# Kernel optimization log

Measured on AMD Instinct MI355X. Metric: run time of the kernel, lower is better.

Reference implementation:

```python
import jax, jax.numpy as jnp
import numpy as np

B, T, D = 128, 512, 400
N_VALS, N_ACTS = 1024, 128

def setup_inputs() -> dict:
    key = jax.random.key(0)
    ks = jax.random.split(key, 7)
    H_utt = jax.random.normal(ks[0], (B, T, D), dtype=jnp.float32)
    c_utt = jax.random.normal(ks[1], (B, D), dtype=jnp.float32)
    C_acts = jax.random.normal(ks[2], (B, N_ACTS, D), dtype=jnp.float32)
    C_vals = jax.random.normal(ks[3], (N_VALS, 1, D), dtype=jnp.float32)
    W_score = jax.random.normal(ks[4], (1, D), dtype=jnp.float32) * (1.0 / np.sqrt(D))
    b_score = jnp.zeros((1,), dtype=jnp.float32)
    lens = jax.random.randint(ks[5], (B,), T // 2, T + 1, dtype=jnp.int64 if jax.config.read('jax_enable_x64') else jnp.int32)
    lens = lens.at[0].set(T)  # ensure max(lens) == T so masking matches torch semantics
    return {"H_utt": H_utt, "c_utt": c_utt, "C_acts": C_acts, "C_vals": C_vals,
            "W_score": W_score, "b_score": b_score, "utterance_len": lens}

def reference(H_utt, c_utt, C_acts, C_vals, W_score, b_score, utterance_len):
    vals = C_vals[:, 0, :]                                   # [V, D]
    # --- y_utts: default attention of each value vector over utterance states ---
    scores = jnp.einsum('btd,vd->bvt', H_utt, vals)          # mul+sum scoring
    mask = jnp.arange(T)[None, :] < utterance_len[:, None]   # [B, T]
    scores = jnp.where(mask[:, None, :], scores, -jnp.inf)
    probs = jax.nn.softmax(scores, axis=-1)                  # [B, V, T]
    q_utts = jnp.einsum('bvt,btd->bvd', probs, H_utt)        # weighted sum contexts
    y_utts = jnp.einsum('bvd,d->bv', q_utts, W_score[0]) + b_score[0]  # utt_scorer
    # --- y_acts: attention of c_utt over per-example act vectors, then score vs vals ---
    s2 = jnp.einsum('bad,bd->ba', C_acts, c_utt)
    p2 = jax.nn.softmax(s2, axis=-1)
    q_acts = jnp.einsum('ba,bad->bd', p2, C_acts)            # [B, D]
    y_acts = q_acts @ vals.T                                 # [B, V]
    return (y_utts, y_acts)
```

## Files before the change

### kernel.cpp

```cpp
#include <hip/hip_runtime.h>
#include <hip/hip_bf16.h>

#define B_  128
#define T_  512
#define D_  400
#define NV  1024
#define NA  128

#define LDH  424
#define NT   32
#define MV   128

typedef __bf16 bf16_t;
typedef bf16_t bf16x8 __attribute__((ext_vector_type(8)));
typedef bf16_t bf16x4 __attribute__((ext_vector_type(4)));
typedef float  floatx4 __attribute__((ext_vector_type(4)));

__device__ inline void async_copy16(const void* g, void* l) {
    __builtin_amdgcn_global_load_lds(
        (const __attribute__((address_space(1))) unsigned int*)g,
        (__attribute__((address_space(3))) unsigned int*)l, 16, 0, 0);
}

__device__ inline float dot4(float4 a, float4 b) {
    return a.x * b.x + a.y * b.y + a.z * b.z + a.w * b.w;
}

__global__ __launch_bounds__(256) void hw_prep_kernel(const float* __restrict__ H,
                                                      const float* __restrict__ W,
                                                      float* __restrict__ hw,
                                                      bf16_t* __restrict__ Hbf) {
    int wave = threadIdx.x >> 6;
    int lane = threadIdx.x & 63;
    long row = (long)blockIdx.x * 4 + wave;
    const float* h = H + row * D_;
    bf16_t* orow = Hbf + row * (long)LDH;
    float acc = 0.f;
    if (lane < 50) {
        const float4* p  = (const float4*)(h + lane * 8);
        const float4* wp = (const float4*)(W + lane * 8);
        float4 x = p[0], y = p[1];
        float4 wx = wp[0], wy = wp[1];
        acc = dot4(x, wx) + dot4(y, wy);
        bf16x8 f;
        f[0] = (bf16_t)x.x; f[1] = (bf16_t)x.y; f[2] = (bf16_t)x.z; f[3] = (bf16_t)x.w;
        f[4] = (bf16_t)y.x; f[5] = (bf16_t)y.y; f[6] = (bf16_t)y.z; f[7] = (bf16_t)y.w;
        *(bf16x8*)(orow + lane * 8) = f;
    } else if (lane < 53) {
        bf16x8 z;
#pragma unroll
        for (int j = 0; j < 8; ++j) z[j] = (bf16_t)0.0f;
        *(bf16x8*)(orow + 400 + (lane - 50) * 8) = z;
    }
#pragma unroll
    for (int off = 1; off < 64; off <<= 1) acc += __shfl_xor(acc, off, 64);
    if (lane == 0) hw[row] = acc;
}

__global__ __launch_bounds__(256) void hw_kernel(const float* __restrict__ H,
                                                 const float* __restrict__ W,
                                                 float* __restrict__ hw) {
    int wave = threadIdx.x >> 6;
    int lane = threadIdx.x & 63;
    long row = (long)blockIdx.x * 4 + wave;
    const float* h = H + row * D_;
    float acc = 0.f;
    for (int k = lane; k < D_; k += 64) acc += h[k] * W[k];
#pragma unroll
    for (int off = 1; off < 64; off <<= 1) acc += __shfl_xor(acc, off, 64);
    if (lane == 0) hw[row] = acc;
}

__global__ __launch_bounds__(256) void qacts_kernel(const float* __restrict__ cu,
                                                    const float* __restrict__ Ca,
                                                    float* __restrict__ q_ws) {
    __shared__ __align__(16) float4 cu4[100];
    __shared__ float s_lds[NA];
    __shared__ float p_lds[NA];
    __shared__ float red[8];
    __shared__ __align__(16) float4 part[100];
    int b = blockIdx.x;
    int tid = threadIdx.x, wave = tid >> 6, lane = tid & 63;

    if (tid < 100) cu4[tid] = ((const float4*)(cu + (size_t)b * D_))[tid];
    __syncthreads();

    const float4* Cb4 = (const float4*)(Ca + (size_t)b * NA * D_);
#pragma unroll 2
    for (int i = 0; i < 32; ++i) {
        int a = wave * 32 + i;
        const float4* row = Cb4 + (size_t)a * 100;
        float acc = dot4(row[lane], cu4[lane]);
        if (lane < 36) acc += dot4(row[lane + 64], cu4[lane + 64]);
#pragma unroll
        for (int off = 1; off < 64; off <<= 1) acc += __shfl_xor(acc, off, 64);
        if (lane == 0) s_lds[a] = acc;
    }
    __syncthreads();

    float s = (tid < NA) ? s_lds[tid] : -3.0e38f;
    float m = s;
#pragma unroll
    for (int off = 1; off < 64; off <<= 1) m = fmaxf(m, __shfl_xor(m, off, 64));
    if (lane == 0) red[wave] = m;
    __syncthreads();
    m = fmaxf(red[0], red[1]);
    float e = (tid < NA) ? __expf(s - m) : 0.f;
    float sum = e;
#pragma unroll
    for (int off = 1; off < 64; off <<= 1) sum += __shfl_xor(sum, off, 64);
    if (lane == 0) red[4 + wave] = sum;
    __syncthreads();
    float S = red[4] + red[5];
    if (tid < NA) p_lds[tid] = e / S;
    __syncthreads();

    int c4 = tid % 100;
    int half = tid / 100;
    float4 acc0 = {0.f, 0.f, 0.f, 0.f};
    if (tid < 200) {
        float4 acc1 = {0.f, 0.f, 0.f, 0.f};
        int a0 = half * 64;
#pragma unroll 4
        for (int a = 0; a < 64; a += 2) {
            float p0 = p_lds[a0 + a], p1 = p_lds[a0 + a + 1];
            float4 x0 = Cb4[(size_t)(a0 + a) * 100 + c4];
            float4 x1 = Cb4[(size_t)(a0 + a + 1) * 100 + c4];
            acc0.x += p0 * x0.x; acc0.y += p0 * x0.y; acc0.z += p0 * x0.z; acc0.w += p0 * x0.w;
            acc1.x += p1 * x1.x; acc1.y += p1 * x1.y; acc1.z += p1 * x1.z; acc1.w += p1 * x1.w;
        }
        acc0.x += acc1.x; acc0.y += acc1.y; acc0.z += acc1.z; acc0.w += acc1.w;
        if (half == 1) part[c4] = acc0;
    }
    __syncthreads();
    if (tid < 100) {
        float4 o = part[c4];
        o.x += acc0.x; o.y += acc0.y; o.z += acc0.z; o.w += acc0.w;
        ((float4*)(q_ws + (size_t)b * D_))[c4] = o;
    }
}

template<int PRE>
__global__ __launch_bounds__(256, 2) void main_kernel(const float* __restrict__ H,
                                                      const bf16_t* __restrict__ Hbf,
                                                      const float* __restrict__ Cv,
                                                      const float* __restrict__ hw,
                                                      const float* __restrict__ q_ws,
                                                      const float* __restrict__ bs,
                                                      const int* __restrict__ lens,
                                                      float* __restrict__ out) {
    __shared__ bf16_t h_lds[2][NT * LDH];

    int i = blockIdx.x;
    int xcd = i & 7, vc = (i >> 3) & 7, bb = i >> 6;
    int b = xcd + 8 * bb;
    int vbase = vc * MV;

    int tid = threadIdx.x;
    int wave = tid >> 6, lane = tid & 63;
    int lrow = lane & 15, quad = lane >> 4;

    int len = lens[b];
    float b0 = bs[0];

    if (!PRE) {
        for (int idx = tid; idx < 2 * NT * (LDH - D_); idx += 256) {
            int bu = idx / (NT * (LDH - D_));
            int rem = idx % (NT * (LDH - D_));
            int r = rem / (LDH - D_), c = rem % (LDH - D_);
            h_lds[bu][r * LDH + D_ + c] = (bf16_t)0.0f;
        }
    }

    bf16x8 afrag[2][13];
#pragma unroll
    for (int set = 0; set < 2; ++set) {
        const float* vrow = Cv + (size_t)(vbase + wave * 32 + set * 16 + lrow) * D_;
#pragma unroll
        for (int kk = 0; kk < 13; ++kk) {
            int k0 = kk * 32 + quad * 8;
            bf16x8 f;
            if (k0 >= D_) {
#pragma unroll
                for (int j = 0; j < 8; ++j) f[j] = (bf16_t)0.0f;
            } else {
                const float4* p = (const float4*)(vrow + k0);
                float4 x = p[0], y = p[1];
                f[0] = (bf16_t)x.x; f[1] = (bf16_t)x.y;
                f[2] = (bf16_t)x.z; f[3] = (bf16_t)x.w;
                f[4] = (bf16_t)y.x; f[5] = (bf16_t)y.y;
                f[6] = (bf16_t)y.z; f[7] = (bf16_t)y.w;
            }
            afrag[set][kk] = f;
        }
    }

    float m_s[2][4], l_s[2][4], a_s[2][4];
#pragma unroll
    for (int set = 0; set < 2; ++set)
#pragma unroll
        for (int r = 0; r < 4; ++r) { m_s[set][r] = -3.0e38f; l_s[set][r] = 0.f; a_s[set][r] = 0.f; }

    int ntiles = (len + NT - 1) / NT;
    const float* Hb = H + (size_t)b * T_ * D_;
    const bf16_t* Hbfb = Hbf + (size_t)b * T_ * LDH;
    const float* hwb = hw + (size_t)b * T_;

    auto stage = [&](int buf, int tt) {
        if (PRE) {
            const char* gt = (const char*)(Hbfb + (size_t)tt * NT * LDH);
            char* lt = (char*)h_lds[buf];
#pragma unroll 1
            for (int off = tid * 16; off < NT * LDH * 2; off += 4096)
                async_copy16(gt + off, lt + off);
        } else {
            for (int idx = tid; idx < NT * (D_ / 4); idx += 256) {
                int r = idx / (D_ / 4), c4 = idx % (D_ / 4);
                float4 x = *(const float4*)(Hb + (size_t)(tt * NT + r) * D_ + c4 * 4);
                bf16x4 f;
                f[0] = (bf16_t)x.x; f[1] = (bf16_t)x.y;
                f[2] = (bf16_t)x.z; f[3] = (bf16_t)x.w;
                *(bf16x4*)(&h_lds[buf][r * LDH + c4 * 4]) = f;
            }
        }
    };

    stage(0, 0);
    __syncthreads();

    for (int tt = 0; tt < ntiles; ++tt) {
        int cur = tt & 1;
        if (tt + 1 < ntiles) stage(cur ^ 1, tt + 1);

        int t0 = tt * NT;
        float hwv[2];
#pragma unroll
        for (int s = 0; s < 2; ++s) hwv[s] = hwb[t0 + s * 16 + lrow];

        floatx4 c[2][2];
        floatx4 zero4 = {0.f, 0.f, 0.f, 0.f};
#pragma unroll
        for (int set = 0; set < 2; ++set)
#pragma unroll
            for (int s = 0; s < 2; ++s) c[set][s] = zero4;

#pragma unroll
        for (int kk = 0; kk < 13; ++kk) {
            int koff = kk * 32 + quad * 8;
#pragma unroll
            for (int s = 0; s < 2; ++s) {
                bf16x8 bfr = *(const bf16x8*)(&h_lds[cur][(s * 16 + lrow) * LDH + koff]);
                c[0][s] = __builtin_amdgcn_mfma_f32_16x16x32_bf16(afrag[0][kk], bfr, c[0][s], 0, 0, 0);
                c[1][s] = __builtin_amdgcn_mfma_f32_16x16x32_bf16(afrag[1][kk], bfr, c[1][s], 0, 0, 0);
            }
        }

        if (t0 + NT > len) {
#pragma unroll
            for (int s = 0; s < 2; ++s) {
                int t = t0 + s * 16 + lrow;
                if (t >= len) {
#pragma unroll
                    for (int set = 0; set < 2; ++set) {
                        c[set][s][0] = -3.0e38f; c[set][s][1] = -3.0e38f;
                        c[set][s][2] = -3.0e38f; c[set][s][3] = -3.0e38f;
                    }
                }
            }
        }

#pragma unroll
        for (int set = 0; set < 2; ++set)
#pragma unroll
            for (int r = 0; r < 4; ++r) {
                float cm = fmaxf(c[set][0][r], c[set][1][r]);
                float mn = fmaxf(m_s[set][r], cm);
                float alpha = __expf(m_s[set][r] - mn);
                float ps = 0.f, qs = 0.f;
#pragma unroll
                for (int s = 0; s < 2; ++s) {
                    float p = __expf(c[set][s][r] - mn);
                    ps += p;
                    qs += p * hwv[s];
                }
                l_s[set][r] = l_s[set][r] * alpha + ps;
                a_s[set][r] = a_s[set][r] * alpha + qs;
                m_s[set][r] = mn;
            }

        __syncthreads();
    }

#pragma unroll
    for (int set = 0; set < 2; ++set)
#pragma unroll
        for (int r = 0; r < 4; ++r) {
            float m = m_s[set][r], l = l_s[set][r], a = a_s[set][r];
#pragma unroll
            for (int off = 1; off < 16; off <<= 1) {
                float mo = __shfl_xor(m, off, 64);
                float lo = __shfl_xor(l, off, 64);
                float ao = __shfl_xor(a, off, 64);
                float mn = fmaxf(m, mo);
                float f1 = __expf(m - mn), f2 = __expf(mo - mn);
                l = l * f1 + lo * f2;
                a = a * f1 + ao * f2;
                m = mn;
            }
            if (lrow == 0) {
                int v = vbase + wave * 32 + set * 16 + quad * 4 + r;
                out[(size_t)b * NV + v] = a / l + b0;
            }
        }

    {
        const float4* q4 = (const float4*)(q_ws + (size_t)b * D_);
        float4 qa = q4[lane];
        float4 qb = (lane < 36) ? q4[lane + 64] : make_float4(0.f, 0.f, 0.f, 0.f);
#pragma unroll 1
        for (int ii = 0; ii < 32; ii += 4) {
            int v0 = vbase + wave * 32 + ii;
            float acc[4];
#pragma unroll
            for (int r = 0; r < 4; ++r) {
                const float4* v4 = (const float4*)(Cv + (size_t)(v0 + r) * D_);
                acc[r] = dot4(v4[lane], qa);
                if (lane < 36) acc[r] += dot4(v4[lane + 64], qb);
            }
#pragma unroll
            for (int off = 1; off < 64; off <<= 1) {
#pragma unroll
                for (int r = 0; r < 4; ++r) acc[r] += __shfl_xor(acc[r], off, 64);
            }
            if (lane == 0) {
                float4 o = make_float4(acc[0], acc[1], acc[2], acc[3]);
                *(float4*)(out + (size_t)B_ * NV + (size_t)b * NV + v0) = o;
            }
        }
    }
}

extern "C" void kernel_launch(void* const* d_in, const int* in_sizes, int n_in,
                              void* d_out, int out_size, void* d_ws, size_t ws_size,
                              hipStream_t stream) {
    const float* H    = (const float*)d_in[0];
    const float* cu   = (const float*)d_in[1];
    const float* Ca   = (const float*)d_in[2];
    const float* Cv   = (const float*)d_in[3];
    const float* W    = (const float*)d_in[4];
    const float* bs   = (const float*)d_in[5];
    const int*   lens = (const int*)d_in[6];
    float* out = (float*)d_out;

    float*  hw   = (float*)d_ws;
    float*  q_ws = hw + (size_t)B_ * T_;
    bf16_t* Hbf  = (bf16_t*)(q_ws + (size_t)B_ * D_);

    size_t need = ((size_t)B_ * T_ + (size_t)B_ * D_) * sizeof(float)
                + (size_t)B_ * T_ * LDH * sizeof(bf16_t);
    bool pre = (ws_size >= need);

    if (pre) {
        hw_prep_kernel<<<dim3(B_ * T_ / 4), dim3(256), 0, stream>>>(H, W, hw, Hbf);
    } else {
        hw_kernel<<<dim3(B_ * T_ / 4), dim3(256), 0, stream>>>(H, W, hw);
    }
    qacts_kernel<<<dim3(B_), dim3(256), 0, stream>>>(cu, Ca, q_ws);
    if (pre) {
        main_kernel<1><<<dim3(1024), dim3(256), 0, stream>>>(H, Hbf, Cv, hw, q_ws, bs, lens, out);
    } else {
        main_kernel<0><<<dim3(1024), dim3(256), 0, stream>>>(H, Hbf, Cv, hw, q_ws, bs, lens, out);
    }
}
```

Before: 316.5 us.

## Swizzle bf16 H tile layout in LDS and shrink row padding

Shrinks the padded row stride of the bf16 H copy from 424 to 416 elements and applies an XOR swizzle of 16-byte chunks keyed on row index, both in the prep kernel's global layout and the fallback LDS staging path. MFMA B-fragment reads apply the matching XOR so the fragment loads avoid LDS bank conflicts with a smaller buffer. The smaller LDS footprint, together with launch bounds raised to 3 blocks per CU, aims for higher occupancy. The risk is register pressure from the tighter launch bound, since each thread holds 26 bf16x8 A fragments.

```diff
diff --git a/kernel.cpp b/kernel.cpp
--- a/kernel.cpp
+++ b/kernel.cpp
@@ -7,7 +7,7 @@
 #define NV  1024
 #define NA  128
 
-#define LDH  424
+#define LDH  416
 #define NT   32
 #define MV   128
 
@@ -33,6 +33,7 @@
     int wave = threadIdx.x >> 6;
     int lane = threadIdx.x & 63;
     long row = (long)blockIdx.x * 4 + wave;
+    int key = (int)(row & 7);
     const float* h = H + row * D_;
     bf16_t* orow = Hbf + row * (long)LDH;
     float acc = 0.f;
@@ -45,12 +46,13 @@
         bf16x8 f;
         f[0] = (bf16_t)x.x; f[1] = (bf16_t)x.y; f[2] = (bf16_t)x.z; f[3] = (bf16_t)x.w;
         f[4] = (bf16_t)y.x; f[5] = (bf16_t)y.y; f[6] = (bf16_t)y.z; f[7] = (bf16_t)y.w;
-        *(bf16x8*)(orow + lane * 8) = f;
-    } else if (lane < 53) {
+        int pos = (lane < 48) ? (lane ^ key) : lane;
+        *(bf16x8*)(orow + pos * 8) = f;
+    } else if (lane < 52) {
         bf16x8 z;
 #pragma unroll
         for (int j = 0; j < 8; ++j) z[j] = (bf16_t)0.0f;
-        *(bf16x8*)(orow + 400 + (lane - 50) * 8) = z;
+        *(bf16x8*)(orow + lane * 8) = z;
     }
 #pragma unroll
     for (int off = 1; off < 64; off <<= 1) acc += __shfl_xor(acc, off, 64);
@@ -141,7 +143,7 @@
 }
 
 template<int PRE>
-__global__ __launch_bounds__(256, 2) void main_kernel(const float* __restrict__ H,
+__global__ __launch_bounds__(256, 3) void main_kernel(const float* __restrict__ H,
                                                       const bf16_t* __restrict__ Hbf,
                                                       const float* __restrict__ Cv,
                                                       const float* __restrict__ hw,
@@ -164,11 +166,13 @@
     float b0 = bs[0];
 
     if (!PRE) {
-        for (int idx = tid; idx < 2 * NT * (LDH - D_); idx += 256) {
-            int bu = idx / (NT * (LDH - D_));
-            int rem = idx % (NT * (LDH - D_));
-            int r = rem / (LDH - D_), c = rem % (LDH - D_);
-            h_lds[bu][r * LDH + D_ + c] = (bf16_t)0.0f;
+        for (int idx = tid; idx < 2 * NT * 2; idx += 256) {
+            int bu = idx >> 6, rem = idx & 63;
+            int r = rem >> 1, c = 50 + (rem & 1);
+            bf16x8 z;
+#pragma unroll
+            for (int j = 0; j < 8; ++j) z[j] = (bf16_t)0.0f;
+            *(bf16x8*)((char*)h_lds[bu] + r * 832 + c * 16) = z;
         }
     }
 
@@ -214,19 +218,27 @@
             for (int off = tid * 16; off < NT * LDH * 2; off += 4096)
                 async_copy16(gt + off, lt + off);
         } else {
-            for (int idx = tid; idx < NT * (D_ / 4); idx += 256) {
-                int r = idx / (D_ / 4), c4 = idx % (D_ / 4);
-                float4 x = *(const float4*)(Hb + (size_t)(tt * NT + r) * D_ + c4 * 4);
-                bf16x4 f;
+            for (int idx = tid; idx < NT * 50; idx += 256) {
+                int r = idx / 50, c = idx % 50;
+                const float4* src = (const float4*)(Hb + (size_t)(tt * NT + r) * D_ + c * 8);
+                float4 x = src[0], y = src[1];
+                bf16x8 f;
                 f[0] = (bf16_t)x.x; f[1] = (bf16_t)x.y;
                 f[2] = (bf16_t)x.z; f[3] = (bf16_t)x.w;
-                *(bf16x4*)(&h_lds[buf][r * LDH + c4 * 4]) = f;
+                f[4] = (bf16_t)y.x; f[5] = (bf16_t)y.y;
+                f[6] = (bf16_t)y.z; f[7] = (bf16_t)y.w;
+                int pos = (c < 48) ? (c ^ (r & 7)) : c;
+                *(bf16x8*)((char*)h_lds[buf] + r * 832 + pos * 16) = f;
             }
         }
     };
 
     stage(0, 0);
     __syncthreads();
+
+    const int swz = (lrow & 7) << 4;
+    const int rowb0 = lrow * 832;
+    const int rowb1 = (16 + lrow) * 832;
 
     for (int tt = 0; tt < ntiles; ++tt) {
         int cur = tt & 1;
@@ -244,15 +256,17 @@
 #pragma unroll
             for (int s = 0; s < 2; ++s) c[set][s] = zero4;
 
+        const char* L = (const char*)h_lds[cur];
 #pragma unroll
         for (int kk = 0; kk < 13; ++kk) {
-            int koff = kk * 32 + quad * 8;
-#pragma unroll
-            for (int s = 0; s < 2; ++s) {
-                bf16x8 bfr = *(const bf16x8*)(&h_lds[cur][(s * 16 + lrow) * LDH + koff]);
-                c[0][s] = __builtin_amdgcn_mfma_f32_16x16x32_bf16(afrag[0][kk], bfr, c[0][s], 0, 0, 0);
-                c[1][s] = __builtin_amdgcn_mfma_f32_16x16x32_bf16(afrag[1][kk], bfr, c[1][s], 0, 0, 0);
-            }
+            int koffb = (kk * 32 + quad * 8) * 2;
+            int o = (kk < 12) ? (koffb ^ swz) : koffb;
+            bf16x8 f0 = *(const bf16x8*)(L + rowb0 + o);
+            c[0][0] = __builtin_amdgcn_mfma_f32_16x16x32_bf16(afrag[0][kk], f0, c[0][0], 0, 0, 0);
+            c[1][0] = __builtin_amdgcn_mfma_f32_16x16x32_bf16(afrag[1][kk], f0, c[1][0], 0, 0, 0);
+            bf16x8 f1 = *(const bf16x8*)(L + rowb1 + o);
+            c[0][1] = __builtin_amdgcn_mfma_f32_16x16x32_bf16(afrag[0][kk], f1, c[0][1], 0, 0, 0);
+            c[1][1] = __builtin_amdgcn_mfma_f32_16x16x32_bf16(afrag[1][kk], f1, c[1][1], 0, 0, 0);
         }
 
         if (t0 + NT > len) {
```

Measured after the change: 360.7 us. +14.0%, slower.

## Merge hw/bf16 prep and q_acts kernels into one launch; use exp2 softmax

Applied to the files above, without the earlier changes.

Folds the H·W / bf16-conversion kernel and the q_acts kernel into a single prep kernel, with blocks 0-127 doing q_acts and the remaining 2048 blocks each handling 32 rows of H (8 per wave). This removes one launch and lets the two independent jobs run concurrently. Separately, the value vectors are pre-scaled by log2(e) when converted to bf16, so the online softmax can use the hardware exp2 instead of __expf. The pre-scaling adds an extra rounding step before the bf16 cast, a small accuracy risk.

```diff
diff --git a/kernel.cpp b/kernel.cpp
--- a/kernel.cpp
+++ b/kernel.cpp
@@ -10,6 +10,7 @@
 #define LDH  424
 #define NT   32
 #define MV   128
+#define LOG2E 1.4426950408889634f
 
 typedef __bf16 bf16_t;
 typedef bf16_t bf16x8 __attribute__((ext_vector_type(8)));
@@ -26,61 +27,71 @@
     return a.x * b.x + a.y * b.y + a.z * b.z + a.w * b.w;
 }
 
-__global__ __launch_bounds__(256) void hw_prep_kernel(const float* __restrict__ H,
-                                                      const float* __restrict__ W,
-                                                      float* __restrict__ hw,
-                                                      bf16_t* __restrict__ Hbf) {
-    int wave = threadIdx.x >> 6;
-    int lane = threadIdx.x & 63;
-    long row = (long)blockIdx.x * 4 + wave;
-    const float* h = H + row * D_;
-    bf16_t* orow = Hbf + row * (long)LDH;
-    float acc = 0.f;
-    if (lane < 50) {
-        const float4* p  = (const float4*)(h + lane * 8);
-        const float4* wp = (const float4*)(W + lane * 8);
-        float4 x = p[0], y = p[1];
-        float4 wx = wp[0], wy = wp[1];
-        acc = dot4(x, wx) + dot4(y, wy);
-        bf16x8 f;
-        f[0] = (bf16_t)x.x; f[1] = (bf16_t)x.y; f[2] = (bf16_t)x.z; f[3] = (bf16_t)x.w;
-        f[4] = (bf16_t)y.x; f[5] = (bf16_t)y.y; f[6] = (bf16_t)y.z; f[7] = (bf16_t)y.w;
-        *(bf16x8*)(orow + lane * 8) = f;
-    } else if (lane < 53) {
-        bf16x8 z;
-#pragma unroll
-        for (int j = 0; j < 8; ++j) z[j] = (bf16_t)0.0f;
-        *(bf16x8*)(orow + 400 + (lane - 50) * 8) = z;
-    }
-#pragma unroll
-    for (int off = 1; off < 64; off <<= 1) acc += __shfl_xor(acc, off, 64);
-    if (lane == 0) hw[row] = acc;
-}
-
-__global__ __launch_bounds__(256) void hw_kernel(const float* __restrict__ H,
-                                                 const float* __restrict__ W,
-                                                 float* __restrict__ hw) {
-    int wave = threadIdx.x >> 6;
-    int lane = threadIdx.x & 63;
-    long row = (long)blockIdx.x * 4 + wave;
-    const float* h = H + row * D_;
-    float acc = 0.f;
-    for (int k = lane; k < D_; k += 64) acc += h[k] * W[k];
-#pragma unroll
-    for (int off = 1; off < 64; off <<= 1) acc += __shfl_xor(acc, off, 64);
-    if (lane == 0) hw[row] = acc;
-}
-
-__global__ __launch_bounds__(256) void qacts_kernel(const float* __restrict__ cu,
-                                                    const float* __restrict__ Ca,
-                                                    float* __restrict__ q_ws) {
+template<int PRE>
+__global__ __launch_bounds__(256) void prep_kernel(const float* __restrict__ H,
+                                                   const float* __restrict__ W,
+                                                   const float* __restrict__ cu,
+                                                   const float* __restrict__ Ca,
+                                                   float* __restrict__ hw,
+                                                   bf16_t* __restrict__ Hbf,
+                                                   float* __restrict__ q_ws) {
     __shared__ __align__(16) float4 cu4[100];
     __shared__ float s_lds[NA];
     __shared__ float p_lds[NA];
     __shared__ float red[8];
     __shared__ __align__(16) float4 part[100];
+
+    int tid = threadIdx.x, wave = tid >> 6, lane = tid & 63;
+
+    if (blockIdx.x >= 128) {
+        long wid = (long)(blockIdx.x - 128) * 4 + wave;
+        long r0 = wid * 8;
+        const float* base = H + r0 * D_;
+        float acc[8];
+#pragma unroll
+        for (int j = 0; j < 8; ++j) acc[j] = 0.f;
+
+        if (lane < 50) {
+            float4 wx = ((const float4*)W)[lane * 2];
+            float4 wy = ((const float4*)W)[lane * 2 + 1];
+            bf16_t* ob = Hbf + r0 * (long)LDH + lane * 8;
+#pragma unroll
+            for (int j = 0; j < 8; ++j) {
+                const float4* p = (const float4*)(base + (long)j * D_ + lane * 8);
+                float4 x = p[0], y = p[1];
+                acc[j] = dot4(x, wx) + dot4(y, wy);
+                if (PRE) {
+                    bf16x8 f;
+                    f[0] = (bf16_t)x.x; f[1] = (bf16_t)x.y;
+                    f[2] = (bf16_t)x.z; f[3] = (bf16_t)x.w;
+                    f[4] = (bf16_t)y.x; f[5] = (bf16_t)y.y;
+                    f[6] = (bf16_t)y.z; f[7] = (bf16_t)y.w;
+                    *(bf16x8*)(ob + (long)j * LDH) = f;
+                }
+            }
+        } else if (PRE && lane < 53) {
+            bf16x8 z;
+#pragma unroll
+            for (int jj = 0; jj < 8; ++jj) z[jj] = (bf16_t)0.0f;
+            bf16_t* ob = Hbf + r0 * (long)LDH + lane * 8;
+#pragma unroll
+            for (int j = 0; j < 8; ++j)
+                *(bf16x8*)(ob + (long)j * LDH) = z;
+        }
+
+#pragma unroll
+        for (int off = 1; off < 64; off <<= 1) {
+#pragma unroll
+            for (int j = 0; j < 8; ++j) acc[j] += __shfl_xor(acc[j], off, 64);
+        }
+        if (lane == 0) {
+#pragma unroll
+            for (int j = 0; j < 8; ++j) hw[r0 + j] = acc[j];
+        }
+        return;
+    }
+
     int b = blockIdx.x;
-    int tid = threadIdx.x, wave = tid >> 6, lane = tid & 63;
 
     if (tid < 100) cu4[tid] = ((const float4*)(cu + (size_t)b * D_))[tid];
     __syncthreads();
@@ -186,10 +197,10 @@
             } else {
                 const float4* p = (const float4*)(vrow + k0);
                 float4 x = p[0], y = p[1];
-                f[0] = (bf16_t)x.x; f[1] = (bf16_t)x.y;
-                f[2] = (bf16_t)x.z; f[3] = (bf16_t)x.w;
-                f[4] = (bf16_t)y.x; f[5] = (bf16_t)y.y;
-                f[6] = (bf16_t)y.z; f[7] = (bf16_t)y.w;
+                f[0] = (bf16_t)(x.x * LOG2E); f[1] = (bf16_t)(x.y * LOG2E);
+                f[2] = (bf16_t)(x.z * LOG2E); f[3] = (bf16_t)(x.w * LOG2E);
+                f[4] = (bf16_t)(y.x * LOG2E); f[5] = (bf16_t)(y.y * LOG2E);
+                f[6] = (bf16_t)(y.z * LOG2E); f[7] = (bf16_t)(y.w * LOG2E);
             }
             afrag[set][kk] = f;
         }
@@ -275,11 +286,11 @@
             for (int r = 0; r < 4; ++r) {
                 float cm = fmaxf(c[set][0][r], c[set][1][r]);
                 float mn = fmaxf(m_s[set][r], cm);
-                float alpha = __expf(m_s[set][r] - mn);
+                float alpha = __builtin_amdgcn_exp2f(m_s[set][r] - mn);
                 float ps = 0.f, qs = 0.f;
 #pragma unroll
                 for (int s = 0; s < 2; ++s) {
-                    float p = __expf(c[set][s][r] - mn);
+                    float p = __builtin_amdgcn_exp2f(c[set][s][r] - mn);
                     ps += p;
                     qs += p * hwv[s];
                 }
@@ -302,7 +313,8 @@
                 float lo = __shfl_xor(l, off, 64);
                 float ao = __shfl_xor(a, off, 64);
                 float mn = fmaxf(m, mo);
-                float f1 = __expf(m - mn), f2 = __expf(mo - mn);
+                float f1 = __builtin_amdgcn_exp2f(m - mn);
+                float f2 = __builtin_amdgcn_exp2f(mo - mn);
                 l = l * f1 + lo * f2;
                 a = a * f1 + ao * f2;
                 m = mn;
@@ -360,15 +372,12 @@
                 + (size_t)B_ * T_ * LDH * sizeof(bf16_t);
     bool pre = (ws_size >= need);
 
+    dim3 pgrid(128 + 2048);
     if (pre) {
-        hw_prep_kernel<<<dim3(B_ * T_ / 4), dim3(256), 0, stream>>>(H, W, hw, Hbf);
-    } else {
-        hw_kernel<<<dim3(B_ * T_ / 4), dim3(256), 0, stream>>>(H, W, hw);
-    }
-    qacts_kernel<<<dim3(B_), dim3(256), 0, stream>>>(cu, Ca, q_ws);
-    if (pre) {
+        prep_kernel<1><<<pgrid, dim3(256), 0, stream>>>(H, W, cu, Ca, hw, Hbf, q_ws);
         main_kernel<1><<<dim3(1024), dim3(256), 0, stream>>>(H, Hbf, Cv, hw, q_ws, bs, lens, out);
     } else {
+        prep_kernel<0><<<pgrid, dim3(256), 0, stream>>>(H, W, cu, Ca, hw, Hbf, q_ws);
         main_kernel<0><<<dim3(1024), dim3(256), 0, stream>>>(H, Hbf, Cv, hw, q_ws, bs, lens, out);
     }
 }
```

Result: faster. 309.7 us (-2.2%).
